# Kernel tuning notes

Hardware: AMD Instinct MI355X
Metric: run time of the kernel (lower is better)

## Reference

```python
import jax, jax.numpy as jnp
import numpy as np


def setup_inputs() -> dict:
    key = jax.random.key(0)
    k1, k2, k3 = jax.random.split(key, 3)
    B, T, H, OUT = 32, 2048, 1024, 256
    hidden_states = jax.random.normal(k1, (B, T, H), dtype=jnp.float32)
    W1 = jax.random.normal(k2, (H, H), dtype=jnp.float32) * (1.0 / np.sqrt(H))
    b1 = jnp.zeros((H,), dtype=jnp.float32)
    Wv = jax.random.normal(k3, (2 * H, OUT), dtype=jnp.float32) * (1.0 / np.sqrt(2 * H))
    bv = jnp.zeros((OUT,), dtype=jnp.float32)
    return {"hidden_states": hidden_states, "W1": W1, "b1": b1, "Wv": Wv, "bv": bv}


def reference(hidden_states, W1, b1, Wv, bv):
    # first_score = Dense(H)(hidden_states): [B,T,H]
    first_score = jnp.einsum('bth,hk->btk', hidden_states, W1) + b1
    # h_t = last timestep of the PROJECTED states: [B,H]
    h_t = first_score[:, -1, :]
    # score = dot([first_score, h_t], [2,1]): [B,T]
    score = jnp.einsum('bth,bh->bt', first_score, h_t)
    attention_weights = jax.nn.softmax(score, axis=-1)  # softmax over T
    # context = dot([hidden_states, weights], [1,1]): contract T -> [B,H]
    context_vector = jnp.einsum('bth,bt->bh', hidden_states, attention_weights)
    pre_activation = jnp.concatenate([context_vector, h_t], axis=-1)  # [B,2H]
    return jnp.tanh(pre_activation @ Wv + bv)  # [B,256]
```

## Files before the change

### kernel.cpp

```cpp
#include <hip/hip_runtime.h>
#include <math.h>

#define B   32
#define T   2048
#define H   1024
#define OUTD 256
#define NC  32
#define KC1 16

__global__ __launch_bounds__(256) void k1a_partial_ht(
    const float* __restrict__ hs, const float* __restrict__ W1,
    float* __restrict__ ph)
{
    const int tid = threadIdx.x;
    const int h   = blockIdx.x * 256 + tid;
    const int k0  = blockIdx.y * 64;

    __shared__ float s_hs[B][64];
    for (int it = 0; it < 8; ++it) {
        int idx = tid + it * 256;
        int b = idx >> 6, k = idx & 63;
        s_hs[b][k] = hs[((size_t)(b * T + (T - 1)) << 10) + k0 + k];
    }
    __syncthreads();

    float acc[B];
#pragma unroll
    for (int b = 0; b < B; ++b) acc[b] = 0.f;

    for (int k4 = 0; k4 < 16; ++k4) {
        float w0 = W1[(size_t)(k0 + k4 * 4 + 0) * H + h];
        float w1 = W1[(size_t)(k0 + k4 * 4 + 1) * H + h];
        float w2 = W1[(size_t)(k0 + k4 * 4 + 2) * H + h];
        float w3 = W1[(size_t)(k0 + k4 * 4 + 3) * H + h];
#pragma unroll
        for (int b = 0; b < B; ++b) {
            const float4 hv = *(const float4*)&s_hs[b][k4 * 4];
            acc[b] = fmaf(hv.x, w0, acc[b]);
            acc[b] = fmaf(hv.y, w1, acc[b]);
            acc[b] = fmaf(hv.z, w2, acc[b]);
            acc[b] = fmaf(hv.w, w3, acc[b]);
        }
    }
    float* dst = ph + ((size_t)blockIdx.y * B << 10);
#pragma unroll
    for (int b = 0; b < B; ++b) dst[((size_t)b << 10) + h] = acc[b];
}

__global__ __launch_bounds__(256) void k1b_reduce_ht(
    const float* __restrict__ ph, const float* __restrict__ b1,
    float* __restrict__ h_t, float* __restrict__ accum)
{
    int i = blockIdx.x * 256 + threadIdx.x;
    int h = i & (H - 1);
    float s = b1[h];
#pragma unroll
    for (int c = 0; c < KC1; ++c)
        s += ph[((size_t)c * B << 10) + i];
    h_t[i] = s;
    if (i < B * OUTD) accum[i] = 0.f;
}

__global__ __launch_bounds__(256) void k2_compute_u(
    const float* __restrict__ W1, const float* __restrict__ h_t,
    float* __restrict__ u)
{
    const int wid  = threadIdx.x >> 6;
    const int lane = threadIdx.x & 63;
    const int k    = blockIdx.x * 4 + wid;
    const float4* wr = (const float4*)(W1 + ((size_t)k << 10));
    float4 wq[4];
#pragma unroll
    for (int j = 0; j < 4; ++j) wq[j] = wr[lane + 64 * j];

    for (int b = 0; b < B; ++b) {
        const float4* hr = (const float4*)(h_t + ((size_t)b << 10));
        float s = 0.f;
#pragma unroll
        for (int j = 0; j < 4; ++j) {
            float4 hv = hr[lane + 64 * j];
            s += wq[j].x * hv.x + wq[j].y * hv.y + wq[j].z * hv.z + wq[j].w * hv.w;
        }
#pragma unroll
        for (int off = 32; off; off >>= 1) s += __shfl_xor(s, off, 64);
        if (lane == 0) u[((size_t)b << 10) + k] = s;
    }
}

__global__ __launch_bounds__(256) void k3_fused(
    const float* __restrict__ hs, const float* __restrict__ u,
    float* __restrict__ ctx_p, float* __restrict__ m_p, float* __restrict__ l_p)
{
    const int c    = blockIdx.x;
    const int b    = blockIdx.y;
    const int w    = threadIdx.x >> 6;
    const int lane = threadIdx.x & 63;
    const int tid  = threadIdx.x;

    const float4* urow = (const float4*)(u + ((size_t)b << 10));
    float4 uq[4];
#pragma unroll
    for (int j = 0; j < 4; ++j) uq[j] = urow[lane + 64 * j];

    const int t0 = c * 64 + w * 16;
    const float4* xrow = (const float4*)(hs + ((size_t)(b * T + t0) << 10));

    float m = -INFINITY, lsum = 0.f;
    float4 acc[4];
#pragma unroll
    for (int j = 0; j < 4; ++j) acc[j] = make_float4(0.f, 0.f, 0.f, 0.f);

    float4 x[4], y[4];
#pragma unroll
    for (int j = 0; j < 4; ++j) x[j] = xrow[lane + 64 * j];

    for (int r = 0; r < 16; ++r) {
        const float4* nrow = xrow + 256;
        if (r < 15) {
#pragma unroll
            for (int j = 0; j < 4; ++j) y[j] = nrow[lane + 64 * j];
        }
        float s = 0.f;
#pragma unroll
        for (int j = 0; j < 4; ++j)
            s += x[j].x * uq[j].x + x[j].y * uq[j].y + x[j].z * uq[j].z + x[j].w * uq[j].w;
#pragma unroll
        for (int off = 32; off; off >>= 1) s += __shfl_xor(s, off, 64);

        float mn = fmaxf(m, s);
        float al = __expf(m - mn);
        float wt = __expf(s - mn);
        lsum = lsum * al + wt;
#pragma unroll
        for (int j = 0; j < 4; ++j) {
            acc[j].x = fmaf(acc[j].x, al, wt * x[j].x);
            acc[j].y = fmaf(acc[j].y, al, wt * x[j].y);
            acc[j].z = fmaf(acc[j].z, al, wt * x[j].z);
            acc[j].w = fmaf(acc[j].w, al, wt * x[j].w);
        }
        m = mn;
#pragma unroll
        for (int j = 0; j < 4; ++j) x[j] = y[j];
        xrow = nrow;
    }

    __shared__ float sm[4], sl[4];
    __shared__ float sacc[4][H];
    if (lane == 0) { sm[w] = m; sl[w] = lsum; }
    __syncthreads();
    const float mp = fmaxf(fmaxf(sm[0], sm[1]), fmaxf(sm[2], sm[3]));
    const float alw = __expf(m - mp);
    float4* sa = (float4*)&sacc[w][0];
#pragma unroll
    for (int j = 0; j < 4; ++j) {
        float4 v;
        v.x = acc[j].x * alw; v.y = acc[j].y * alw;
        v.z = acc[j].z * alw; v.w = acc[j].w * alw;
        sa[lane + 64 * j] = v;
    }
    __syncthreads();
    float lp = 0.f;
#pragma unroll
    for (int ww = 0; ww < 4; ++ww) lp += sl[ww] * __expf(sm[ww] - mp);

    float* dst = ctx_p + (((size_t)b * NC + c) << 10);
#pragma unroll
    for (int i = 0; i < 4; ++i) {
        int h = tid + 256 * i;
        dst[h] = sacc[0][h] + sacc[1][h] + sacc[2][h] + sacc[3][h];
    }
    if (tid == 0) { m_p[b * NC + c] = mp; l_p[b * NC + c] = lp; }
}

__global__ __launch_bounds__(256) void k45_matmul(
    const float* __restrict__ ctx_p, const float* __restrict__ m_p,
    const float* __restrict__ l_p, const float* __restrict__ h_t,
    const float* __restrict__ Wv, float* __restrict__ accum)
{
    const int kc = blockIdx.x;
    const int b  = blockIdx.y;
    const int o  = threadIdx.x;

    __shared__ float sp[256];
    if (kc < 4) {
        float M = -INFINITY;
#pragma unroll
        for (int c = 0; c < NC; ++c) M = fmaxf(M, m_p[b * NC + c]);
        float L = 0.f;
#pragma unroll
        for (int c = 0; c < NC; ++c) L += l_p[b * NC + c] * __expf(m_p[b * NC + c] - M);
        float s = 0.f;
#pragma unroll
        for (int c = 0; c < NC; ++c)
            s += ctx_p[(((size_t)b * NC + c) << 10) + kc * 256 + o]
                 * __expf(m_p[b * NC + c] - M);
        sp[o] = s / L;
    } else {
        sp[o] = h_t[((size_t)b << 10) + (kc - 4) * 256 + o];
    }
    __syncthreads();

    float acc = 0.f;
    const float* wv = Wv + (size_t)kc * 256 * OUTD + o;
#pragma unroll 8
    for (int k = 0; k < 256; ++k)
        acc = fmaf(sp[k], wv[(size_t)k * OUTD], acc);
    atomicAdd(&accum[b * OUTD + o], acc);
}

__global__ __launch_bounds__(256) void k5b_tanh(
    const float* __restrict__ accum, const float* __restrict__ bv,
    float* __restrict__ out)
{
    int i = blockIdx.x * 256 + threadIdx.x;
    out[i] = tanhf(accum[i] + bv[i & (OUTD - 1)]);
}

extern "C" void kernel_launch(void* const* d_in, const int* in_sizes, int n_in,
                              void* d_out, int out_size, void* d_ws, size_t ws_size,
                              hipStream_t stream)
{
    const float* hs = (const float*)d_in[0];
    const float* W1 = (const float*)d_in[1];
    const float* b1 = (const float*)d_in[2];
    const float* Wv = (const float*)d_in[3];
    const float* bv = (const float*)d_in[4];
    float* out = (float*)d_out;
    float* ws  = (float*)d_ws;

    float* ph    = ws;
    float* h_t   = ph + (size_t)KC1 * B * H;
    float* u     = h_t + (size_t)B * H;
    float* m_p   = u + (size_t)B * H;
    float* l_p   = m_p + B * NC;
    float* ctx_p = l_p + B * NC;
    float* accum = ctx_p + (size_t)B * NC * H;

    k1a_partial_ht<<<dim3(4, KC1), 256, 0, stream>>>(hs, W1, ph);
    k1b_reduce_ht<<<(B * H) / 256, 256, 0, stream>>>(ph, b1, h_t, accum);
    k2_compute_u<<<H / 4, 256, 0, stream>>>(W1, h_t, u);
    k3_fused<<<dim3(NC, B), 256, 0, stream>>>(hs, u, ctx_p, m_p, l_p);
    k45_matmul<<<dim3(8, B), 256, 0, stream>>>(ctx_p, m_p, l_p, h_t, Wv, accum);
    k5b_tanh<<<B, 256, 0, stream>>>(accum, bv, out);
}
```

Measured before the change: 429.2 us.

## Fuse final matmul with tanh, deepen k3 prefetch, batch k2 shuffle reductions

Merges the output matmul, the softmax-normalisation combine and the tanh into a single 1024-thread block per batch. This removes the atomicAdd accumulation, the accum zeroing and one kernel launch. The fused streaming kernel now prefetches two rows ahead instead of one, and the u computation defers all 32 wave reductions so the shuffles can be interleaved. The trade-offs are higher register pressure in k2 and k3, and only 32 blocks for the final stage.

```diff
diff --git a/kernel.cpp b/kernel.cpp
--- a/kernel.cpp
+++ b/kernel.cpp
@@ -49,7 +49,7 @@
 
 __global__ __launch_bounds__(256) void k1b_reduce_ht(
     const float* __restrict__ ph, const float* __restrict__ b1,
-    float* __restrict__ h_t, float* __restrict__ accum)
+    float* __restrict__ h_t)
 {
     int i = blockIdx.x * 256 + threadIdx.x;
     int h = i & (H - 1);
@@ -58,7 +58,6 @@
     for (int c = 0; c < KC1; ++c)
         s += ph[((size_t)c * B << 10) + i];
     h_t[i] = s;
-    if (i < B * OUTD) accum[i] = 0.f;
 }
 
 __global__ __launch_bounds__(256) void k2_compute_u(
@@ -73,17 +72,26 @@
 #pragma unroll
     for (int j = 0; j < 4; ++j) wq[j] = wr[lane + 64 * j];
 
+    float s[B];
+#pragma unroll 8
     for (int b = 0; b < B; ++b) {
         const float4* hr = (const float4*)(h_t + ((size_t)b << 10));
-        float s = 0.f;
+        float t = 0.f;
 #pragma unroll
         for (int j = 0; j < 4; ++j) {
             float4 hv = hr[lane + 64 * j];
-            s += wq[j].x * hv.x + wq[j].y * hv.y + wq[j].z * hv.z + wq[j].w * hv.w;
-        }
-#pragma unroll
-        for (int off = 32; off; off >>= 1) s += __shfl_xor(s, off, 64);
-        if (lane == 0) u[((size_t)b << 10) + k] = s;
+            t += wq[j].x * hv.x + wq[j].y * hv.y + wq[j].z * hv.z + wq[j].w * hv.w;
+        }
+        s[b] = t;
+    }
+#pragma unroll
+    for (int off = 32; off; off >>= 1) {
+#pragma unroll
+        for (int b = 0; b < B; ++b) s[b] += __shfl_xor(s[b], off, 64);
+    }
+    if (lane == 0) {
+#pragma unroll
+        for (int b = 0; b < B; ++b) u[((size_t)b << 10) + k] = s[b];
     }
 }
 
@@ -103,22 +111,23 @@
     for (int j = 0; j < 4; ++j) uq[j] = urow[lane + 64 * j];
 
     const int t0 = c * 64 + w * 16;
-    const float4* xrow = (const float4*)(hs + ((size_t)(b * T + t0) << 10));
+    const float4* base = (const float4*)(hs + ((size_t)(b * T + t0) << 10));
 
     float m = -INFINITY, lsum = 0.f;
     float4 acc[4];
 #pragma unroll
     for (int j = 0; j < 4; ++j) acc[j] = make_float4(0.f, 0.f, 0.f, 0.f);
 
-    float4 x[4], y[4];
-#pragma unroll
-    for (int j = 0; j < 4; ++j) x[j] = xrow[lane + 64 * j];
+    float4 x[4], y[4], z[4];
+#pragma unroll
+    for (int j = 0; j < 4; ++j) x[j] = base[lane + 64 * j];
+#pragma unroll
+    for (int j = 0; j < 4; ++j) y[j] = base[256 + lane + 64 * j];
 
     for (int r = 0; r < 16; ++r) {
-        const float4* nrow = xrow + 256;
-        if (r < 15) {
-#pragma unroll
-            for (int j = 0; j < 4; ++j) y[j] = nrow[lane + 64 * j];
+        if (r < 14) {
+#pragma unroll
+            for (int j = 0; j < 4; ++j) z[j] = base[(r + 2) * 256 + lane + 64 * j];
         }
         float s = 0.f;
 #pragma unroll
@@ -140,8 +149,7 @@
         }
         m = mn;
 #pragma unroll
-        for (int j = 0; j < 4; ++j) x[j] = y[j];
-        xrow = nrow;
+        for (int j = 0; j < 4; ++j) { x[j] = y[j]; y[j] = z[j]; }
     }
 
     __shared__ float sm[4], sl[4];
@@ -172,48 +180,47 @@
     if (tid == 0) { m_p[b * NC + c] = mp; l_p[b * NC + c] = lp; }
 }
 
-__global__ __launch_bounds__(256) void k45_matmul(
+__global__ __launch_bounds__(1024) void k46_out(
     const float* __restrict__ ctx_p, const float* __restrict__ m_p,
     const float* __restrict__ l_p, const float* __restrict__ h_t,
-    const float* __restrict__ Wv, float* __restrict__ accum)
-{
-    const int kc = blockIdx.x;
-    const int b  = blockIdx.y;
-    const int o  = threadIdx.x;
-
-    __shared__ float sp[256];
-    if (kc < 4) {
-        float M = -INFINITY;
-#pragma unroll
-        for (int c = 0; c < NC; ++c) M = fmaxf(M, m_p[b * NC + c]);
-        float L = 0.f;
-#pragma unroll
-        for (int c = 0; c < NC; ++c) L += l_p[b * NC + c] * __expf(m_p[b * NC + c] - M);
-        float s = 0.f;
-#pragma unroll
-        for (int c = 0; c < NC; ++c)
-            s += ctx_p[(((size_t)b * NC + c) << 10) + kc * 256 + o]
-                 * __expf(m_p[b * NC + c] - M);
-        sp[o] = s / L;
-    } else {
-        sp[o] = h_t[((size_t)b << 10) + (kc - 4) * 256 + o];
-    }
+    const float* __restrict__ Wv, const float* __restrict__ bv,
+    float* __restrict__ out)
+{
+    const int b   = blockIdx.x;
+    const int tid = threadIdx.x;
+    const int o   = tid & 255;
+    const int q   = tid >> 8;
+
+    __shared__ float sp[2 * H];
+    __shared__ float red[4][OUTD];
+
+    float M = -INFINITY;
+#pragma unroll
+    for (int c = 0; c < NC; ++c) M = fmaxf(M, m_p[b * NC + c]);
+    float L = 0.f;
+#pragma unroll
+    for (int c = 0; c < NC; ++c) L += l_p[b * NC + c] * __expf(m_p[b * NC + c] - M);
+
+    float s = 0.f;
+#pragma unroll
+    for (int c = 0; c < NC; ++c)
+        s += ctx_p[(((size_t)b * NC + c) << 10) + tid] * __expf(m_p[b * NC + c] - M);
+    sp[tid] = s / L;
+    sp[H + tid] = h_t[((size_t)b << 10) + tid];
     __syncthreads();
 
     float acc = 0.f;
-    const float* wv = Wv + (size_t)kc * 256 * OUTD + o;
+    const float* wv = Wv + ((size_t)q * 512) * OUTD + o;
+    const float* pq = sp + q * 512;
 #pragma unroll 8
-    for (int k = 0; k < 256; ++k)
-        acc = fmaf(sp[k], wv[(size_t)k * OUTD], acc);
-    atomicAdd(&accum[b * OUTD + o], acc);
-}
-
-__global__ __launch_bounds__(256) void k5b_tanh(
-    const float* __restrict__ accum, const float* __restrict__ bv,
-    float* __restrict__ out)
-{
-    int i = blockIdx.x * 256 + threadIdx.x;
-    out[i] = tanhf(accum[i] + bv[i & (OUTD - 1)]);
+    for (int k = 0; k < 512; ++k)
+        acc = fmaf(pq[k], wv[(size_t)k * OUTD], acc);
+    red[q][o] = acc;
+    __syncthreads();
+
+    if (tid < OUTD)
+        out[b * OUTD + tid] = tanhf(red[0][tid] + red[1][tid] + red[2][tid]
+                                    + red[3][tid] + bv[tid]);
 }
 
 extern "C" void kernel_launch(void* const* d_in, const int* in_sizes, int n_in,
@@ -234,12 +241,10 @@
     float* m_p   = u + (size_t)B * H;
     float* l_p   = m_p + B * NC;
     float* ctx_p = l_p + B * NC;
-    float* accum = ctx_p + (size_t)B * NC * H;
 
     k1a_partial_ht<<<dim3(4, KC1), 256, 0, stream>>>(hs, W1, ph);
-    k1b_reduce_ht<<<(B * H) / 256, 256, 0, stream>>>(ph, b1, h_t, accum);
+    k1b_reduce_ht<<<(B * H) / 256, 256, 0, stream>>>(ph, b1, h_t);
     k2_compute_u<<<H / 4, 256, 0, stream>>>(W1, h_t, u);
     k3_fused<<<dim3(NC, B), 256, 0, stream>>>(hs, u, ctx_p, m_p, l_p);
-    k45_matmul<<<dim3(8, B), 256, 0, stream>>>(ctx_p, m_p, l_p, h_t, Wv, accum);
-    k5b_tanh<<<B, 256, 0, stream>>>(accum, bv, out);
-}
+    k46_out<<<B, 1024, 0, stream>>>(ctx_p, m_p, l_p, h_t, Wv, bv, out);
+}
```

Result: slower. 445.2 us (+3.7%).
